# Optimization experiments

Measured on AMD Instinct MI355X. Metric: run time of the kernel, lower is better.

## Reference

```python
import jax, jax.numpy as jnp
import numpy as np

N_SAMPLES = 131072
N_FEATURES = 64
N_TREES = 64
DEPTH = 12                      # complete binary trees
N_INTERNAL = 2 ** DEPTH - 1     # 4095 internal nodes per tree
N_LEAVES = 2 ** DEPTH           # 4096 leaves per tree
N_CLASSES = 8


def setup_inputs() -> dict:
    key = jax.random.key(0)
    k1, k2, k3, k4 = jax.random.split(key, 4)
    X = jax.random.normal(k1, (N_SAMPLES, N_FEATURES), dtype=jnp.float32)
    # flattened complete-binary-tree parameters (FIL-style layout)
    features = jax.random.randint(k2, (N_TREES, N_INTERNAL), 0, N_FEATURES, dtype=jnp.int32)
    thresholds = jax.random.normal(k3, (N_TREES, N_INTERNAL), dtype=jnp.float32)
    leaf_values = jax.random.randint(k4, (N_TREES, N_LEAVES), 0, N_CLASSES, dtype=jnp.int32)
    return {"X": X, "features": features, "thresholds": thresholds, "leaf_values": leaf_values}


def reference(X, features, thresholds, leaf_values):
    # X: [N, F]; features/thresholds: [T, 2^D-1]; leaf_values: [T, 2^D]
    N = X.shape[0]
    row = jnp.arange(N)[None, :]                      # [1, N] broadcasts over trees
    node = jnp.zeros((N_TREES, N), dtype=jnp.int32)   # all samples start at root of every tree
    for _ in range(DEPTH):                            # fixed-depth traversal, fully vectorized
        f = jnp.take_along_axis(features, node, axis=1)      # [T, N] feature id per (tree, sample)
        t = jnp.take_along_axis(thresholds, node, axis=1)    # [T, N]
        xv = X[row, f]                                        # [T, N] gathered feature values
        node = 2 * node + 1 + (xv > t).astype(jnp.int32)      # go left (<=) or right (>)
    leaf_idx = node - N_INTERNAL                              # [T, N] in [0, 2^D)
    preds = jnp.take_along_axis(leaf_values, leaf_idx, axis=1)  # [T, N] per-tree class votes
    # majority vote == torch.mode over trees; argmax returns smallest class on ties,
    # matching torch.mode's smallest-modal-value convention
    counts = (preds[:, :, None] == jnp.arange(N_CLASSES)[None, None, :]).sum(axis=0)  # [N, C]
    return jnp.argmax(counts, axis=1)  # [N] final class predictions
```

## Files before the change

### kernel.cpp

```cpp
#include <hip/hip_runtime.h>


constexpr int kSamples  = 131072;
constexpr int kFeat     = 64;
constexpr int kTrees    = 64;
constexpr int kInternal = 4095;
constexpr int kClasses  = 8;

constexpr int TPB  = 1024;
constexpr int SPB  = 256;
constexpr int XSTR = 256;
constexpr int XLDS_BYTES = kFeat * XSTR * 4;
constexpr int ILP  = 8;
constexpr int TREES_PER_THREAD = 16;

struct Pair  { float thr0, thrL, thrR; unsigned meta; };
struct Sub16 { float thr10, thrL, thrR; unsigned meta; };

constexpr int kPairItems = kTrees * 341;
constexpr int kSubItems  = kTrees * 1024;
constexpr int kPackItems = kPairItems + kSubItems;


__global__ __launch_bounds__(256) void pack_kernel(
    const int* __restrict__ features, const float* __restrict__ thresholds,
    const int* __restrict__ leaf_values,
    Pair* __restrict__ pairsA, Sub16* __restrict__ subsA)
{
    int g = blockIdx.x * 256 + threadIdx.x;
    if (g < kPairItems) {
        int t = g / 341;
        int e = g - t * 341;
        int p, m;
        if      (e < 1)  { p = 0; m = e; }
        else if (e < 5)  { p = 1; m = e - 1; }
        else if (e < 21) { p = 2; m = e - 5; }
        else if (e < 85) { p = 3; m = e - 21; }
        else             { p = 4; m = e - 85; }
        int g0 = (1 << (2 * p)) - 1 + m;
        int b  = t * kInternal;
        Pair pr;
        pr.thr0 = thresholds[b + g0];
        pr.thrL = thresholds[b + 2 * g0 + 1];
        pr.thrR = thresholds[b + 2 * g0 + 2];
        pr.meta = (unsigned)features[b + g0]
                | ((unsigned)features[b + 2 * g0 + 1] << 6)
                | ((unsigned)features[b + 2 * g0 + 2] << 12);
        pairsA[(t << 9) + e] = pr;
    } else if (g < kPackItems) {
        int i2 = g - kPairItems;
        int t = i2 >> 10;
        int j = i2 & 1023;
        int n10 = 1023 + j;
        int b   = t * kInternal;
        Sub16 sb;
        sb.thr10 = thresholds[b + n10];
        sb.thrL  = thresholds[b + 2 * n10 + 1];
        sb.thrR  = thresholds[b + 2 * n10 + 2];
        const int* lv = leaf_values + ((t << 12) + 4 * j);
        sb.meta = (unsigned)features[b + n10]
                | ((unsigned)features[b + 2 * n10 + 1] << 6)
                | ((unsigned)features[b + 2 * n10 + 2] << 12)
                | ((unsigned)lv[0] << 18) | ((unsigned)lv[1] << 21)
                | ((unsigned)lv[2] << 24) | ((unsigned)lv[3] << 27);
        subsA[(t << 10) + j] = sb;
    }
}


__global__ __launch_bounds__(TPB, 8) void forest_kernel(
    const float* __restrict__ X,
    const Pair*  __restrict__ pairsA,
    const Sub16* __restrict__ subsA,
    int* __restrict__ out)
{
    extern __shared__ float xs[];
    const int tid  = threadIdx.x;
    const int s    = tid & (SPB - 1);
    const int h    = tid >> 8;
    const int base = blockIdx.x * SPB;

    {
        const float4* Xr = (const float4*)(X + (size_t)(base + s) * kFeat) + h * 4;
        #pragma unroll
        for (int k = 0; k < 4; ++k) {
            float4 v = Xr[k];
            int f0 = (h * 4 + k) * 4;
            xs[(f0 + 0) * XSTR + s] = v.x;
            xs[(f0 + 1) * XSTR + s] = v.y;
            xs[(f0 + 2) * XSTR + s] = v.z;
            xs[(f0 + 3) * XSTR + s] = v.w;
        }
    }
    __syncthreads();

    const char* xb = (const char*)xs + (s << 2);
    unsigned long long votes = 0ull;

    const int mofs[4] = {0, 1, 5, 21};

    const int tbeg = h * TREES_PER_THREAD;
    for (int t0 = tbeg; t0 < tbeg + TREES_PER_THREAD; t0 += ILP) {
        int m[ILP];
        #pragma unroll
        for (int j = 0; j < ILP; ++j) m[j] = 0;

        #pragma unroll
        for (int p = 0; p < 4; ++p) {
            #pragma unroll
            for (int j = 0; j < ILP; ++j) {
                Pair pr = pairsA[((t0 + j) << 9) + mofs[p] + m[j]];
                float x0 = *(const float*)(xb + ((pr.meta & 63u) << 10));
                int c0 = x0 > pr.thr0 ? 1 : 0;
                float thr1     = c0 ? pr.thrR : pr.thrL;
                unsigned fsel  = c0 ? (pr.meta >> 12) : (pr.meta >> 6);
                float x1 = *(const float*)(xb + ((fsel & 63u) << 10));
                int c1 = x1 > thr1 ? 1 : 0;
                m[j] = 4 * m[j] + 2 * c0 + c1;
            }
        }

        #pragma unroll
        for (int j = 0; j < ILP; ++j) {
            Pair pr = pairsA[((t0 + j) << 9) + 85 + m[j]];
            float x0 = *(const float*)(xb + ((pr.meta & 63u) << 10));
            int c0 = x0 > pr.thr0 ? 1 : 0;
            float thr1     = c0 ? pr.thrR : pr.thrL;
            unsigned fsel  = c0 ? (pr.meta >> 12) : (pr.meta >> 6);
            float x1 = *(const float*)(xb + ((fsel & 63u) << 10));
            int c1 = x1 > thr1 ? 1 : 0;
            m[j] = 4 * m[j] + 2 * c0 + c1;
        }

        #pragma unroll
        for (int j = 0; j < ILP; ++j) {
            Sub16 sb = subsA[((t0 + j) << 10) + m[j]];
            unsigned mt = sb.meta;
            float x0 = *(const float*)(xb + ((mt & 63u) << 10));
            int c0 = x0 > sb.thr10 ? 1 : 0;
            float thr1    = c0 ? sb.thrR : sb.thrL;
            unsigned fsel = c0 ? (mt >> 12) : (mt >> 6);
            float x1 = *(const float*)(xb + ((fsel & 63u) << 10));
            int c1 = x1 > thr1 ? 1 : 0;
            int cls = (mt >> (18 + 3 * ((c0 << 1) | c1))) & 7;
            votes += 1ull << (cls << 3);
        }
    }

    __syncthreads();
    unsigned long long* vbuf = (unsigned long long*)xs;
    if (h != 0) vbuf[(h - 1) * SPB + s] = votes;
    __syncthreads();
    if (h == 0) {
        votes += vbuf[s] + vbuf[SPB + s] + vbuf[2 * SPB + s];
        int best = 0;
        int bc   = (int)(votes & 0xFFull);
        #pragma unroll
        for (int c = 1; c < kClasses; ++c) {
            int cnt = (int)((votes >> (c * 8)) & 0xFFull);
            if (cnt > bc) { bc = cnt; best = c; }
        }
        out[base + s] = best;
    }
}

extern "C" void kernel_launch(void* const* d_in, const int* in_sizes, int n_in,
                              void* d_out, int out_size, void* d_ws, size_t ws_size,
                              hipStream_t stream) {
    const float* X          = (const float*)d_in[0];
    const int*   features   = (const int*)d_in[1];
    const float* thresholds = (const float*)d_in[2];
    const int*   leaves     = (const int*)d_in[3];
    int*         out        = (int*)d_out;

    Pair*  pairsA = (Pair*)d_ws;
    Sub16* subsA  = (Sub16*)((char*)d_ws + (kTrees << 13));

    (void)hipFuncSetAttribute((const void*)forest_kernel,
                              hipFuncAttributeMaxDynamicSharedMemorySize,
                              XLDS_BYTES);

    pack_kernel<<<(kPackItems + 255) / 256, 256, 0, stream>>>(
        features, thresholds, leaves, pairsA, subsA);
    forest_kernel<<<kSamples / SPB, TPB, XLDS_BYTES, stream>>>(
        X, pairsA, subsA, out);
}
```

Baseline: 116.6 us.

## Stage top-tree pair nodes in LDS per window of four trees

Copies the packed pair nodes of the first ten tree levels into shared memory, for four trees per thread group at a time. Traversal of those levels then reads nodes from LDS instead of global memory, and the window is refilled between tree groups with block barriers. Per-thread tree ILP drops from eight to four. The larger LDS footprint limits residency to one block per CU, and the added barriers reduce overlap.

```diff
diff --git a/kernel.cpp b/kernel.cpp
--- a/kernel.cpp
+++ b/kernel.cpp
@@ -11,8 +11,12 @@
 constexpr int SPB  = 256;
 constexpr int XSTR = 256;
 constexpr int XLDS_BYTES = kFeat * XSTR * 4;
-constexpr int ILP  = 8;
 constexpr int TREES_PER_THREAD = 16;
+constexpr int WTREES = 4;
+constexpr int NWIN   = TREES_PER_THREAD / WTREES;
+constexpr int PTREE  = 344;
+constexpr int PAIR_LDS_BYTES = 4 * WTREES * PTREE * 16;
+constexpr int TOTAL_LDS = XLDS_BYTES + PAIR_LDS_BYTES;
 
 struct Pair  { float thr0, thrL, thrR; unsigned meta; };
 struct Sub16 { float thr10, thrL, thrR; unsigned meta; };
@@ -68,17 +72,22 @@
 }
 
 
-__global__ __launch_bounds__(TPB, 8) void forest_kernel(
+__global__ __launch_bounds__(TPB, 1) void forest_kernel(
     const float* __restrict__ X,
     const Pair*  __restrict__ pairsA,
     const Sub16* __restrict__ subsA,
     int* __restrict__ out)
 {
-    extern __shared__ float xs[];
+    extern __shared__ char lds[];
+    float* xs = (float*)lds;
+    Pair*  pl = (Pair*)(lds + XLDS_BYTES);
+
     const int tid  = threadIdx.x;
     const int s    = tid & (SPB - 1);
     const int h    = tid >> 8;
     const int base = blockIdx.x * SPB;
+
+    Pair* plh = pl + h * (WTREES * PTREE);
 
     {
         const float4* Xr = (const float4*)(X + (size_t)(base + s) * kFeat) + h * 4;
@@ -92,6 +101,16 @@
             xs[(f0 + 3) * XSTR + s] = v.w;
         }
     }
+
+    {
+        const Pair* src = pairsA + ((h * TREES_PER_THREAD) << 9);
+        #pragma unroll
+        for (int tr = 0; tr < WTREES; ++tr) {
+            plh[tr * PTREE + s] = src[(tr << 9) + s];
+            int e2 = s + 256;
+            if (e2 < PTREE) plh[tr * PTREE + e2] = src[(tr << 9) + e2];
+        }
+    }
     __syncthreads();
 
     const char* xb = (const char*)xs + (s << 2);
@@ -99,17 +118,18 @@
 
     const int mofs[4] = {0, 1, 5, 21};
 
-    const int tbeg = h * TREES_PER_THREAD;
-    for (int t0 = tbeg; t0 < tbeg + TREES_PER_THREAD; t0 += ILP) {
-        int m[ILP];
-        #pragma unroll
-        for (int j = 0; j < ILP; ++j) m[j] = 0;
+    for (int w = 0; w < NWIN; ++w) {
+        const int t0 = h * TREES_PER_THREAD + w * WTREES;
+
+        int m[WTREES];
+        #pragma unroll
+        for (int j = 0; j < WTREES; ++j) m[j] = 0;
 
         #pragma unroll
         for (int p = 0; p < 4; ++p) {
             #pragma unroll
-            for (int j = 0; j < ILP; ++j) {
-                Pair pr = pairsA[((t0 + j) << 9) + mofs[p] + m[j]];
+            for (int j = 0; j < WTREES; ++j) {
+                Pair pr = plh[j * PTREE + mofs[p] + m[j]];
                 float x0 = *(const float*)(xb + ((pr.meta & 63u) << 10));
                 int c0 = x0 > pr.thr0 ? 1 : 0;
                 float thr1     = c0 ? pr.thrR : pr.thrL;
@@ -121,8 +141,8 @@
         }
 
         #pragma unroll
-        for (int j = 0; j < ILP; ++j) {
-            Pair pr = pairsA[((t0 + j) << 9) + 85 + m[j]];
+        for (int j = 0; j < WTREES; ++j) {
+            Pair pr = plh[j * PTREE + 85 + m[j]];
             float x0 = *(const float*)(xb + ((pr.meta & 63u) << 10));
             int c0 = x0 > pr.thr0 ? 1 : 0;
             float thr1     = c0 ? pr.thrR : pr.thrL;
@@ -133,7 +153,7 @@
         }
 
         #pragma unroll
-        for (int j = 0; j < ILP; ++j) {
+        for (int j = 0; j < WTREES; ++j) {
             Sub16 sb = subsA[((t0 + j) << 10) + m[j]];
             unsigned mt = sb.meta;
             float x0 = *(const float*)(xb + ((mt & 63u) << 10));
@@ -145,6 +165,19 @@
             int cls = (mt >> (18 + 3 * ((c0 << 1) | c1))) & 7;
             votes += 1ull << (cls << 3);
         }
+
+        if (w + 1 < NWIN) {
+            __syncthreads();
+            const Pair* src = pairsA +
+                ((h * TREES_PER_THREAD + (w + 1) * WTREES) << 9);
+            #pragma unroll
+            for (int tr = 0; tr < WTREES; ++tr) {
+                plh[tr * PTREE + s] = src[(tr << 9) + s];
+                int e2 = s + 256;
+                if (e2 < PTREE) plh[tr * PTREE + e2] = src[(tr << 9) + e2];
+            }
+            __syncthreads();
+        }
     }
 
     __syncthreads();
@@ -178,10 +211,10 @@
 
     (void)hipFuncSetAttribute((const void*)forest_kernel,
                               hipFuncAttributeMaxDynamicSharedMemorySize,
-                              XLDS_BYTES);
+                              TOTAL_LDS);
 
     pack_kernel<<<(kPackItems + 255) / 256, 256, 0, stream>>>(
         features, thresholds, leaves, pairsA, subsA);
-    forest_kernel<<<kSamples / SPB, TPB, XLDS_BYTES, stream>>>(
+    forest_kernel<<<kSamples / SPB, TPB, TOTAL_LDS, stream>>>(
         X, pairsA, subsA, out);
 }
```

Result: slower. 133.3 us (+14.3%).
